# Performance work log

Measured on AMD Instinct MI355X. Metric: run time of the kernel, lower is better.

The kernel has to match this reference:

```python
import jax, jax.numpy as jnp
import numpy as np

HID = 1024   # hidden_dim
H = 16       # num_head
D = 64       # head_dim
W = 64       # window_size (one-sided attention radius)


def setup_inputs() -> dict:
    key = jax.random.key(0)
    ks = jax.random.split(key, 10)
    B, S = 2, 4096
    s = 0.02
    X = jax.random.normal(ks[0], (B, S, HID), jnp.float32)
    mask = jnp.ones((B, S), jnp.float32)
    Wq = jax.random.normal(ks[1], (HID, H * D), jnp.float32) * s
    bq = jnp.zeros((H * D,), jnp.float32)
    Wk = jax.random.normal(ks[2], (HID, H * D), jnp.float32) * s
    bk = jnp.zeros((H * D,), jnp.float32)
    Wv = jax.random.normal(ks[3], (HID, H * D), jnp.float32) * s
    bv = jnp.zeros((H * D,), jnp.float32)
    Wo = jax.random.normal(ks[4], (H * D, HID), jnp.float32) * s
    bo = jnp.zeros((HID,), jnp.float32)
    return dict(X=X, mask=mask, Wq=Wq, bq=bq, Wk=Wk, bk=bk, Wv=Wv, bv=bv, Wo=Wo, bo=bo)


def _chunk3(T, nC):
    # T: [B,H,S,D] -> [B,H,nC,3W,D]: for chunk c, keys of chunks c-1, c, c+1 (zero-padded at ends)
    B, Hh, S, Dd = T.shape
    Tp = jnp.pad(T, ((0, 0), (0, 0), (W, W), (0, 0))).reshape(B, Hh, nC + 2, W, Dd)
    return jnp.concatenate([Tp[:, :, :-2], Tp[:, :, 1:-1], Tp[:, :, 2:]], axis=3)


def reference(X, mask, Wq, bq, Wk, bk, Wv, bv, Wo, bo):
    B, S0, _ = X.shape
    pad = W - S0 % W  # matches torch: always >= 1 (full window if divisible)
    Xp = jnp.pad(X, ((0, 0), (0, pad), (0, 0)))
    mp = jnp.pad(mask, ((0, 0), (0, pad)))  # padded keys masked out
    S = S0 + pad
    nC = S // W

    def proj(Wm, b):
        return (Xp @ Wm + b).reshape(B, S, H, D).transpose(0, 2, 1, 3)  # [B,H,S,D]

    Q, K, V = proj(Wq, bq), proj(Wk, bk), proj(Wv, bv)
    Qc = Q.reshape(B, H, nC, W, D)
    K3 = _chunk3(K, nC)
    V3 = _chunk3(V, nC)

    # banded scores: query i attends keys j with |i - j| <= W
    scores = jnp.einsum('bhcqd,bhckd->bhcqk', Qc, K3) / jnp.asarray(np.sqrt(D), jnp.float32)
    qi = jnp.arange(W)[:, None]
    kj = jnp.arange(3 * W)[None, :]
    band = (kj >= qi) & (kj <= qi + 2 * W)  # [W, 3W]
    m3 = jnp.pad(mp, ((0, 0), (W, W))).reshape(B, nC + 2, W)
    m3 = jnp.concatenate([m3[:, :-2], m3[:, 1:-1], m3[:, 2:]], axis=2)  # [B,nC,3W]
    valid = band[None, None, None, :, :] & (m3[:, None, :, None, :] > 0)
    scores = jnp.where(valid, scores, -1e9)
    A = jax.nn.softmax(scores, axis=-1)
    ctx = jnp.einsum('bhcqk,bhckd->bhcqd', A, V3).reshape(B, H, S, D)
    out = ctx.transpose(0, 2, 1, 3).reshape(B, S, H * D) @ Wo + bo
    return out[:, :S0]
```

## Files before the change

### kernel.cpp

```cpp
#include <hip/hip_runtime.h>

typedef unsigned short u16;
typedef unsigned int u32;
typedef __bf16 bf16x8 __attribute__((ext_vector_type(8)));
typedef u16 u16x8 __attribute__((ext_vector_type(8)));
typedef float floatx4 __attribute__((ext_vector_type(4)));

#define MFMA16(a, b, c) __builtin_amdgcn_mfma_f32_16x16x32_bf16((a), (b), (c), 0, 0, 0)

#define B_ 2
#define S0 4096
#define NH 16
#define HD 64
#define HID 1024
#define VSTR 216

__device__ __forceinline__ float bf2f(u16 u) {
  union { u32 i; float f; } x; x.i = ((u32)u) << 16; return x.f;
}
__device__ __forceinline__ u16 f2bf(float f) {
  union { float f; u32 i; } x; x.f = f;
  u32 r = x.i + 0x7FFFu + ((x.i >> 16) & 1u);
  return (u16)(r >> 16);
}

__device__ __forceinline__ void glds16(const u16* g, u16* l) {
  __builtin_amdgcn_global_load_lds(
      (const __attribute__((address_space(1))) u32*)g,
      (__attribute__((address_space(3))) u32*)l, 16, 0, 0);
}

__global__ __launch_bounds__(256) void prep(
    const float* __restrict__ X, const float* __restrict__ mask,
    const float* __restrict__ Wq, const float* __restrict__ bq,
    const float* __restrict__ Wk, const float* __restrict__ bk,
    const float* __restrict__ Wv, const float* __restrict__ bv,
    const float* __restrict__ Wo, const float* __restrict__ bo,
    u16* __restrict__ cX, u16* __restrict__ cmask, u16* __restrict__ cb,
    u16* __restrict__ WqkvT, u16* __restrict__ WoT) {
  __shared__ u16 tile[64][66];
  int bid = blockIdx.x;
  if (bid < 4096) {
    int i = (bid * 256 + threadIdx.x) * 8;
    u16x8 v;
#pragma unroll
    for (int j = 0; j < 8; j++) v[j] = f2bf(X[i + j]);
    *(u16x8*)(cX + i) = v;
  } else if (bid < 4144) {
    int tid = (bid - 4096) * 256 + threadIdx.x;
    if (tid < B_ * S0) {
      cmask[tid] = f2bf(mask[tid]);
    } else {
      int j = tid - B_ * S0;
      int seg = j >> 10, idx = j & 1023;
      const float* src = (seg == 0) ? bq : (seg == 1) ? bk : (seg == 2) ? bv : bo;
      cb[seg * 1024 + idx] = f2bf(src[idx]);
    }
  } else {
    int idx = bid - 4144;
    int mat = idx >> 8;
    const float* src = (mat == 0) ? Wq : (mat == 1) ? Wk : (mat == 2) ? Wv : Wo;
    u16* dst = (mat < 3) ? (WqkvT + (size_t)mat * HID * HID) : WoT;
    int t0 = ((idx >> 4) & 15) * 64;
    int c0 = (idx & 15) * 64;
    int tx = threadIdx.x & 63, ty = threadIdx.x >> 6;
#pragma unroll
    for (int i = 0; i < 16; i++) {
      int r = i * 4 + ty;
      tile[r][tx] = f2bf(src[(size_t)(t0 + r) * HID + c0 + tx]);
    }
    __syncthreads();
#pragma unroll
    for (int i = 0; i < 16; i++) {
      int r = i * 4 + ty;
      dst[(size_t)(c0 + r) * HID + t0 + tx] = tile[tx][r];
    }
  }
}

template <int BN, int MODE>
__global__ __launch_bounds__(256) void gemm_bf16_tn(
    const u16* __restrict__ A, const u16* __restrict__ Bt,
    const u16* __restrict__ cb, void* __restrict__ outp, int K) {
  constexpr int NT = BN / 32;
  __shared__ alignas(16) u16 sA[128 * 64];
  __shared__ alignas(16) u16 sB[BN * 64];
  int t = threadIdx.x;
  int wave = t >> 6, lane = t & 63;
  int wm = wave >> 1, wn = wave & 1;
  int quad = lane >> 4, l16 = lane & 15;
  int tile_m = blockIdx.x * 128;
  int tile_n = blockIdx.y * BN;

  floatx4 acc[4][NT] = {};

  int row_l = lane >> 3;
  int col_l = ((lane & 7) ^ row_l) * 8;
  const u16* Ag = A + (size_t)(tile_m + wave * 8 + row_l) * K + col_l;
  const u16* Bg = Bt + (size_t)(tile_n + wave * 8 + row_l) * K + col_l;
  u16* lA = sA + wave * 8 * 64;
  u16* lB = sB + wave * 8 * 64;

  for (int k0 = 0; k0 < K; k0 += 64) {
    __syncthreads();
#pragma unroll
    for (int r = 0; r < 4; r++)
      glds16(Ag + (size_t)(r * 32) * K + k0, lA + r * 2048);
#pragma unroll
    for (int r = 0; r < BN / 32; r++)
      glds16(Bg + (size_t)(r * 32) * K + k0, lB + r * 2048);
    __syncthreads();

#pragma unroll
    for (int ks = 0; ks < 2; ks++) {
      bf16x8 af[4], bfr[NT];
#pragma unroll
      for (int mt = 0; mt < 4; mt++) {
        int row = wm * 64 + mt * 16 + l16;
        int p = (ks * 4 + quad) ^ (row & 7);
        af[mt] = *(const bf16x8*)(sA + row * 64 + p * 8);
      }
#pragma unroll
      for (int nt = 0; nt < NT; nt++) {
        int row = wn * (BN / 2) + nt * 16 + l16;
        int p = (ks * 4 + quad) ^ (row & 7);
        bfr[nt] = *(const bf16x8*)(sB + row * 64 + p * 8);
      }
#pragma unroll
      for (int mt = 0; mt < 4; mt++)
#pragma unroll
        for (int nt = 0; nt < NT; nt++)
          acc[mt][nt] = MFMA16(af[mt], bfr[nt], acc[mt][nt]);
    }
  }

  if (MODE == 0) {
    u16* op = (u16*)outp;
#pragma unroll
    for (int mt = 0; mt < 4; mt++) {
      int row0 = tile_m + wm * 64 + mt * 16 + quad * 4;
      int bb = row0 >> 12;
      int sbase = row0 & (S0 - 1);
#pragma unroll
      for (int nt = 0; nt < NT; nt++) {
        int col = tile_n + wn * (BN / 2) + nt * 16 + l16;
        int p = col >> 10;
        int rem = col & 1023;
        float bias = bf2f(cb[p * 1024 + rem]);
        int hh = rem >> 6, dd = rem & 63;
        u16* dp = op + ((size_t)(((p * 2 + bb) * NH + hh)) * S0 + sbase) * HD + dd;
#pragma unroll
        for (int r = 0; r < 4; r++)
          dp[(size_t)r * HD] = f2bf(acc[mt][nt][r] + bias);
      }
    }
  } else {
    float* op = (float*)outp;
#pragma unroll
    for (int mt = 0; mt < 4; mt++) {
      int row0 = tile_m + wm * 64 + mt * 16 + quad * 4;
#pragma unroll
      for (int nt = 0; nt < NT; nt++) {
        int col = tile_n + wn * (BN / 2) + nt * 16 + l16;
        float bias = bf2f(cb[3 * 1024 + col]);
        float* dp = op + (size_t)row0 * HID + col;
#pragma unroll
        for (int r = 0; r < 4; r++)
          dp[(size_t)r * HID] = acc[mt][nt][r] + bias;
      }
    }
  }
}

__global__ __launch_bounds__(256) void attn_win(
    const u16* __restrict__ Q, const u16* __restrict__ Kp,
    const u16* __restrict__ Vp, const u16* __restrict__ cmask,
    u16* __restrict__ ctx) {
  __shared__ alignas(16) u16 buf0[64 * VSTR];
  __shared__ alignas(16) u16 sP[4 * 16 * 200];
  __shared__ u16 sMk[208];

  int bid = blockIdx.x;
  int c = bid & 63;
  int h = (bid >> 6) & 15;
  int b = bid >> 10;
  int t = threadIdx.x;
  int wave = t >> 6, lane = t & 63;
  int quad = lane >> 4, l16 = lane & 15;
  int koff = wave * 16;

  const u16* Qb = Q + (size_t)(b * NH + h) * S0 * HD;
  const u16* Kb = Kp + (size_t)(b * NH + h) * S0 * HD;
  const u16* Vb = Vp + (size_t)(b * NH + h) * S0 * HD;
  int kbase = (c - 1) * 64;

  int rrow = lane >> 3;
  int csrc = ((lane & 7) ^ rrow) * 8;
#pragma unroll
  for (int p = 0; p < 7; p++) {
    int sl0 = p * 32 + wave * 8;
    if (sl0 < 208) {
      int key = kbase + sl0 + rrow;
      int kc = key < 0 ? 0 : (key > S0 - 1 ? S0 - 1 : key);
      glds16(Kb + (size_t)kc * HD + csrc, buf0 + sl0 * 64);
    }
  }
  if (t < 208) {
    int j = kbase + t;
    sMk[t] = (j >= 0 && j < S0) ? cmask[(size_t)b * S0 + j] : (u16)0;
  }

  int qrow = c * 64 + wave * 16 + l16;
  bf16x8 aqv[2];
#pragma unroll
  for (int ks = 0; ks < 2; ks++)
    aqv[ks] = *(const bf16x8*)(Qb + (size_t)qrow * HD + ks * 32 + quad * 8);

  __syncthreads();

  floatx4 sc[9] = {};
  __builtin_amdgcn_s_setprio(1);
#pragma unroll
  for (int ks = 0; ks < 2; ks++) {
#pragma unroll
    for (int nt = 0; nt < 9; nt++) {
      int slot = koff + nt * 16 + l16;
      int pch = ((ks * 4 + quad) ^ (l16 & 7)) * 8;
      bf16x8 bk = *(const bf16x8*)(buf0 + slot * 64 + pch);
      sc[nt] = MFMA16(aqv[ks], bk, sc[nt]);
    }
  }
  __builtin_amdgcn_s_setprio(0);

  u16x8 vreg[7];
#pragma unroll
  for (int i = 0; i < 7; i++) {
    int e = i * 256 + t;
    if (e < 1664) {
      int dg = e / 208;
      int slot = e - dg * 208;
      int key = kbase + slot;
      int kc = key < 0 ? 0 : (key > S0 - 1 ? S0 - 1 : key);
      vreg[i] = *(const u16x8*)(Vb + (size_t)kc * HD + dg * 8);
    }
  }

  int qrel_base = wave * 16 + quad * 4;
  u16* myP = sP + wave * 16 * 200;
  float kmask[9];
#pragma unroll
  for (int nt = 0; nt < 9; nt++) kmask[nt] = bf2f(sMk[koff + nt * 16 + l16]);

#pragma unroll
  for (int reg = 0; reg < 4; reg++) {
    int qrel = qrel_base + reg;
    float v[9];
    float m = -3e38f;
#pragma unroll
    for (int nt = 0; nt < 9; nt++) {
      int slot = koff + nt * 16 + l16;
      bool ok = (slot >= qrel) && (slot <= qrel + 128) && (kmask[nt] > 0.f);
      float s = ok ? sc[nt][reg] * 0.125f : -1e30f;
      v[nt] = s;
      m = fmaxf(m, s);
    }
#pragma unroll
    for (int off = 1; off <= 8; off <<= 1) m = fmaxf(m, __shfl_xor(m, off));
    float sum = 0.f;
#pragma unroll
    for (int nt = 0; nt < 9; nt++) {
      float p = __expf(v[nt] - m);
      v[nt] = p;
      sum += p;
    }
#pragma unroll
    for (int off = 1; off <= 8; off <<= 1) sum += __shfl_xor(sum, off);
    float inv = 1.0f / sum;
    int prow = (quad * 4 + reg) * 200;
#pragma unroll
    for (int nt = 0; nt < 9; nt++)
      myP[prow + nt * 16 + l16] = f2bf(v[nt] * inv);
    myP[prow + 144 + l16] = 0;
  }
  __syncthreads();

#pragma unroll
  for (int i = 0; i < 7; i++) {
    int e = i * 256 + t;
    if (e < 1664) {
      int dg = e / 208;
      int slot = e - dg * 208;
#pragma unroll
      for (int j = 0; j < 8; j++) buf0[(dg * 8 + j) * VSTR + slot] = vreg[i][j];
    }
  }
  __syncthreads();

  floatx4 oc[4] = {};
  __builtin_amdgcn_s_setprio(1);
#pragma unroll
  for (int ks = 0; ks < 5; ks++) {
    bf16x8 ap = *(const bf16x8*)(myP + l16 * 200 + ks * 32 + quad * 8);
#pragma unroll
    for (int nt = 0; nt < 4; nt++) {
      bf16x8 bv =
          *(const bf16x8*)(buf0 + (nt * 16 + l16) * VSTR + koff + ks * 32 + quad * 8);
      oc[nt] = MFMA16(ap, bv, oc[nt]);
    }
  }
  __builtin_amdgcn_s_setprio(0);

  int srow = c * 64 + wave * 16 + quad * 4;
#pragma unroll
  for (int nt = 0; nt < 4; nt++) {
    u16* dp = ctx + (size_t)(b * S0 + srow) * HID + h * HD + nt * 16 + l16;
#pragma unroll
    for (int reg = 0; reg < 4; reg++)
      dp[(size_t)reg * HID] = f2bf(oc[nt][reg]);
  }
}

extern "C" void kernel_launch(void* const* d_in, const int* in_sizes, int n_in,
                              void* d_out, int out_size, void* d_ws, size_t ws_size,
                              hipStream_t stream) {
  const float* X = (const float*)d_in[0];
  const float* mask = (const float*)d_in[1];
  const float* Wq = (const float*)d_in[2];
  const float* bq = (const float*)d_in[3];
  const float* Wk = (const float*)d_in[4];
  const float* bk = (const float*)d_in[5];
  const float* Wv = (const float*)d_in[6];
  const float* bv = (const float*)d_in[7];
  const float* Wo = (const float*)d_in[8];
  const float* bo = (const float*)d_in[9];
  char* ws = (char*)d_ws;

  const size_t MB = 1048576;
  u16* cmask = (u16*)(ws + 256);
  u16* cb = (u16*)(ws + 256 + 16384);
  u16* cX = (u16*)(ws + 1 * MB);
  u16* WqkvT = (u16*)(ws + 17 * MB);
  u16* WoT = (u16*)(ws + 23 * MB);
  u16* QKV = (u16*)(ws + 25 * MB);
  u16* CTX = cX;

  const size_t per_qkv = (size_t)B_ * NH * S0 * HD;

  prep<<<4096 + 48 + 1024, 256, 0, stream>>>(X, mask, Wq, bq, Wk, bk, Wv, bv,
                                             Wo, bo, cX, cmask, cb, WqkvT, WoT);
  gemm_bf16_tn<128, 0><<<dim3(64, 24), 256, 0, stream>>>(cX, WqkvT, cb, QKV, HID);
  attn_win<<<dim3(B_ * NH * 64), 256, 0, stream>>>(QKV, QKV + per_qkv,
                                                   QKV + 2 * per_qkv, cmask, CTX);
  gemm_bf16_tn<128, 1><<<dim3(64, 8), 256, 0, stream>>>(CTX, WoT, cb, d_out, HID);
}
```

Baseline: 229.7 us.

## Retile QKV GEMM with N-major grid, vectorize X cast, simplify attention LDS

The QKV projection GEMM now uses a 128x96 tile and an N-major block order, giving a 32x64 grid instead of 64x24. The aim is more blocks and better L2 reuse of X rows. The X-to-bf16 conversion now reads float4 vectors. The attention kernel drops the padded V stride (216 to 208), loads Q inside the loop after the barrier, and removes the s_setprio hints. These changes risk LDS bank conflicts on the transposed V reads, and the BN=96 tiling must line up with the unseen load and store code.

```diff
diff --git a/kernel.cpp b/kernel.cpp
--- a/kernel.cpp
+++ b/kernel.cpp
@@ -13,7 +13,6 @@
 #define NH 16
 #define HD 64
 #define HID 1024
-#define VSTR 216
 
 __device__ __forceinline__ float bf2f(u16 u) {
   union { u32 i; float f; } x; x.i = ((u32)u) << 16; return x.f;
@@ -42,9 +41,11 @@
   int bid = blockIdx.x;
   if (bid < 4096) {
     int i = (bid * 256 + threadIdx.x) * 8;
+    const float4* Xv = (const float4*)(X + i);
+    float4 a = Xv[0], b = Xv[1];
     u16x8 v;
-#pragma unroll
-    for (int j = 0; j < 8; j++) v[j] = f2bf(X[i + j]);
+    v[0] = f2bf(a.x); v[1] = f2bf(a.y); v[2] = f2bf(a.z); v[3] = f2bf(a.w);
+    v[4] = f2bf(b.x); v[5] = f2bf(b.y); v[6] = f2bf(b.z); v[7] = f2bf(b.w);
     *(u16x8*)(cX + i) = v;
   } else if (bid < 4144) {
     int tid = (bid - 4096) * 256 + threadIdx.x;
@@ -78,7 +79,7 @@
   }
 }
 
-template <int BN, int MODE>
+template <int BN, int MODE, int NMAJOR>
 __global__ __launch_bounds__(256) void gemm_bf16_tn(
     const u16* __restrict__ A, const u16* __restrict__ Bt,
     const u16* __restrict__ cb, void* __restrict__ outp, int K) {
@@ -89,8 +90,8 @@
   int wave = t >> 6, lane = t & 63;
   int wm = wave >> 1, wn = wave & 1;
   int quad = lane >> 4, l16 = lane & 15;
-  int tile_m = blockIdx.x * 128;
-  int tile_n = blockIdx.y * BN;
+  int tile_m = (NMAJOR ? blockIdx.y : blockIdx.x) * 128;
+  int tile_n = (NMAJOR ? blockIdx.x : blockIdx.y) * BN;
 
   floatx4 acc[4][NT] = {};
 
@@ -176,7 +177,7 @@
     const u16* __restrict__ Q, const u16* __restrict__ Kp,
     const u16* __restrict__ Vp, const u16* __restrict__ cmask,
     u16* __restrict__ ctx) {
-  __shared__ alignas(16) u16 buf0[64 * VSTR];
+  __shared__ alignas(16) u16 buf0[208 * 64];
   __shared__ alignas(16) u16 sP[4 * 16 * 200];
   __shared__ u16 sMk[208];
 
@@ -209,28 +210,21 @@
     int j = kbase + t;
     sMk[t] = (j >= 0 && j < S0) ? cmask[(size_t)b * S0 + j] : (u16)0;
   }
-
+  __syncthreads();
+
+  floatx4 sc[9] = {};
   int qrow = c * 64 + wave * 16 + l16;
-  bf16x8 aqv[2];
-#pragma unroll
-  for (int ks = 0; ks < 2; ks++)
-    aqv[ks] = *(const bf16x8*)(Qb + (size_t)qrow * HD + ks * 32 + quad * 8);
-
-  __syncthreads();
-
-  floatx4 sc[9] = {};
-  __builtin_amdgcn_s_setprio(1);
 #pragma unroll
   for (int ks = 0; ks < 2; ks++) {
+    bf16x8 aq = *(const bf16x8*)(Qb + (size_t)qrow * HD + ks * 32 + quad * 8);
 #pragma unroll
     for (int nt = 0; nt < 9; nt++) {
       int slot = koff + nt * 16 + l16;
       int pch = ((ks * 4 + quad) ^ (l16 & 7)) * 8;
       bf16x8 bk = *(const bf16x8*)(buf0 + slot * 64 + pch);
-      sc[nt] = MFMA16(aqv[ks], bk, sc[nt]);
-    }
-  }
-  __builtin_amdgcn_s_setprio(0);
+      sc[nt] = MFMA16(aq, bk, sc[nt]);
+    }
+  }
 
   u16x8 vreg[7];
 #pragma unroll
@@ -291,24 +285,22 @@
       int dg = e / 208;
       int slot = e - dg * 208;
 #pragma unroll
-      for (int j = 0; j < 8; j++) buf0[(dg * 8 + j) * VSTR + slot] = vreg[i][j];
+      for (int j = 0; j < 8; j++) buf0[(dg * 8 + j) * 208 + slot] = vreg[i][j];
     }
   }
   __syncthreads();
 
   floatx4 oc[4] = {};
-  __builtin_amdgcn_s_setprio(1);
 #pragma unroll
   for (int ks = 0; ks < 5; ks++) {
     bf16x8 ap = *(const bf16x8*)(myP + l16 * 200 + ks * 32 + quad * 8);
 #pragma unroll
     for (int nt = 0; nt < 4; nt++) {
       bf16x8 bv =
-          *(const bf16x8*)(buf0 + (nt * 16 + l16) * VSTR + koff + ks * 32 + quad * 8);
+          *(const bf16x8*)(buf0 + (nt * 16 + l16) * 208 + koff + ks * 32 + quad * 8);
       oc[nt] = MFMA16(ap, bv, oc[nt]);
     }
   }
-  __builtin_amdgcn_s_setprio(0);
 
   int srow = c * 64 + wave * 16 + quad * 4;
 #pragma unroll
@@ -348,8 +340,8 @@
 
   prep<<<4096 + 48 + 1024, 256, 0, stream>>>(X, mask, Wq, bq, Wk, bk, Wv, bv,
                                              Wo, bo, cX, cmask, cb, WqkvT, WoT);
-  gemm_bf16_tn<128, 0><<<dim3(64, 24), 256, 0, stream>>>(cX, WqkvT, cb, QKV, HID);
+  gemm_bf16_tn<96, 0, 1><<<dim3(32, 64), 256, 0, stream>>>(cX, WqkvT, cb, QKV, HID);
   attn_win<<<dim3(B_ * NH * 64), 256, 0, stream>>>(QKV, QKV + per_qkv,
                                                    QKV + 2 * per_qkv, cmask, CTX);
-  gemm_bf16_tn<128, 1><<<dim3(64, 8), 256, 0, stream>>>(CTX, WoT, cb, d_out, HID);
-}
+  gemm_bf16_tn<128, 1, 0><<<dim3(64, 8), 256, 0, stream>>>(CTX, WoT, cb, d_out, HID);
+}
```

Result: no change. 226.2 us (-1.5%).
